# Kernel optimization log

Measured on AMD Instinct MI355X. Metric: run time of the kernel, lower is better.

Reference implementation:

```python
import jax, jax.numpy as jnp
import numpy as np
from jax import lax

C = 8          # bargs.channel
S = 1024       # bargs.test_sidelen
SIGMA = 1.0    # edge_sigma
KS = int(6 * SIGMA + 1)   # 7
PAD = KS // 2             # 3
BW = S // 6               # border_width
LAM, MU, TH = 5.0, 5.0, 1e-4


def _edge_kernel():
    coords = jnp.arange(KS, dtype=jnp.float32) - (KS - 1.0) / 2.0
    g1 = jnp.exp(-coords ** 2 / (2.0 * SIGMA ** 2))
    g1 = g1 / g1.sum()
    g2 = jnp.outer(g1, g1)
    return jnp.broadcast_to(g2, (C, 1, KS, KS))  # depthwise OIHW


def _alpha():
    # max applicable loop index among {row-dist, col-dist}; interior stays 1.
    r = jnp.arange(S)
    g = jnp.where(r < BW, r, jnp.where(S - 1 - r < BW, S - 1 - r, -1))  # [S]
    m = jnp.maximum(g[:, None], g[None, :])                              # [S,S]
    a = jnp.where(m >= 0, m.astype(jnp.float32) / BW, 1.0)
    return a[None, None]  # [1,1,S,S] broadcasts over channels


def _grad_spectrum():
    gv = jnp.array([[-1., -2., -1.], [0., 0., 0.], [1., 2., 1.]], jnp.float32)
    gh = gv.T
    gvf = jnp.fft.fft2(gv, s=(S, S))
    ghf = jnp.fft.fft2(gh, s=(S, S))
    return (jnp.abs(gvf) ** 2 + jnp.abs(ghf) ** 2).astype(jnp.float32)  # real


def _edge_blur(img, kernel, alpha):
    blurred = lax.conv_general_dilated(
        img, kernel, window_strides=(1, 1), padding=[(PAD, PAD), (PAD, PAD)],
        feature_group_count=C, dimension_numbers=('NCHW', 'OIHW', 'NCHW'))
    return alpha * img + (1.0 - alpha) * blurred


def setup_inputs() -> dict:
    key = jax.random.key(0)
    k1, k2 = jax.random.split(key)
    lms = jax.random.uniform(k1, (1, C, S, S), dtype=jnp.float32)
    fuse = jax.random.uniform(k2, (1, C, S, S), dtype=jnp.float32)
    return {"lms": lms, "fuse": fuse}


def reference(lms, fuse):
    kernel = _edge_kernel()
    alpha = _alpha()
    grad = _grad_spectrum()

    lms_fft = jnp.fft.fft2(_edge_blur(lms, kernel, alpha))
    fuse_fft = jnp.fft.fft2(_edge_blur(fuse, kernel, alpha))

    denom = jnp.abs(fuse_fft) ** 2 + LAM + MU * grad      # real [1,C,S,S]
    numer = jnp.conj(fuse_fft) * lms_fft
    psf = jnp.fft.fftshift(jnp.real(jnp.fft.ifft2(numer / denom)), axes=(-2, -1))
    psf = jnp.where(psf < TH, 0.0, psf)                   # [1,C,S,S]

    def crop(p):  # p: [S,S]
        row, col = jnp.unravel_index(jnp.argmax(p), p.shape)
        patch = lax.dynamic_slice(p, (row - 20, col - 20), (41, 41))
        return patch / jnp.sum(patch)

    psf_l = jax.vmap(crop)(psf[0])        # [C,41,41]
    return psf_l[:, None]                 # [C,1,41,41]
```

## Files before the change

kernel.cpp:

```cpp
#include <hip/hip_runtime.h>
#include <math.h>

#define SS 1024
#define NC 8
#define BWD 170
#define THRESH 1e-4f

typedef unsigned long long ull;

__device__ __forceinline__ float2 cmul(float2 a, float2 b) {
    return make_float2(a.x * b.x - a.y * b.y, a.x * b.y + a.y * b.x);
}

#define XS(a) ((a) ^ (((a) >> 4) & 15))

__device__ __forceinline__ int cmap(int kx) {
    if (kx == 0) return 0;
    if (kx == 512) return 1;
    return (kx < 512) ? (kx << 1) : (((1024 - kx) << 1) | 1);
}

template <int DIR>
__device__ __forceinline__ void bfly4(const float2 v[4], float2 r[4]) {
    float2 a = v[0], b = v[1], c = v[2], d = v[3];
    float2 apc = make_float2(a.x + c.x, a.y + c.y);
    float2 amc = make_float2(a.x - c.x, a.y - c.y);
    float2 bpd = make_float2(b.x + d.x, b.y + d.y);
    float2 jb  = make_float2(-(b.y - d.y), b.x - d.x);
    r[0] = make_float2(apc.x + bpd.x, apc.y + bpd.y);
    r[2] = make_float2(apc.x - bpd.x, apc.y - bpd.y);
    if (DIR == -1) {
        r[1] = make_float2(amc.x - jb.x, amc.y - jb.y);
        r[3] = make_float2(amc.x + jb.x, amc.y + jb.y);
    } else {
        r[1] = make_float2(amc.x + jb.x, amc.y + jb.y);
        r[3] = make_float2(amc.x - jb.x, amc.y - jb.y);
    }
}

template <int DIR>
__device__ __forceinline__ void fft1024_reg(float2 v[4], float2* A, float2* B,
                                            int tid, bool sb) {
    float2* dst = A;
    float2* alt = B;
    #pragma unroll
    for (int t = 0; t < 4; ++t) {
        int s = 1 << (2 * t);
        int k = tid & ~(s - 1);
        float2 r[4];
        bfly4<DIR>(v, r);
        float rev = (float)k * (1.0f / 1024.0f);
        float2 w1 = make_float2(__builtin_amdgcn_cosf(rev),
                                (float)DIR * __builtin_amdgcn_sinf(rev));
        float2 w2 = cmul(w1, w1);
        float2 w3 = cmul(w2, w1);
        int base = tid + 3 * k;
        dst[XS(base)]         = r[0];
        dst[XS(base + s)]     = cmul(r[1], w1);
        dst[XS(base + 2 * s)] = cmul(r[2], w2);
        dst[XS(base + 3 * s)] = cmul(r[3], w3);
        __syncthreads();
        v[0] = dst[XS(tid)];
        v[1] = dst[XS(tid + 256)];
        v[2] = dst[XS(tid + 512)];
        v[3] = dst[XS(tid + 768)];
        if (sb) __syncthreads();
        float2* tmp = dst; dst = alt; alt = tmp;
    }
    float2 r[4];
    bfly4<DIR>(v, r);
    v[0] = r[0]; v[1] = r[1]; v[2] = r[2]; v[3] = r[3];
}

template <int DIR>
__device__ __forceinline__ void fft1024_pair(float2 vA[4], float2 vB[4],
                                             float2* A0, float2* A1,
                                             float2* B0, float2* B1,
                                             int tid, bool sb) {
    float2 *dA = A0, *aA = A1, *dB = B0, *aB = B1;
    #pragma unroll
    for (int t = 0; t < 4; ++t) {
        int s = 1 << (2 * t);
        int k = tid & ~(s - 1);
        float rev = (float)k * (1.0f / 1024.0f);
        float2 w1 = make_float2(__builtin_amdgcn_cosf(rev),
                                (float)DIR * __builtin_amdgcn_sinf(rev));
        float2 w2 = cmul(w1, w1);
        float2 w3 = cmul(w2, w1);
        int base = tid + 3 * k;
        float2 rA[4], rB[4];
        bfly4<DIR>(vA, rA);
        bfly4<DIR>(vB, rB);
        dA[XS(base)]         = rA[0];
        dA[XS(base + s)]     = cmul(rA[1], w1);
        dA[XS(base + 2 * s)] = cmul(rA[2], w2);
        dA[XS(base + 3 * s)] = cmul(rA[3], w3);
        dB[XS(base)]         = rB[0];
        dB[XS(base + s)]     = cmul(rB[1], w1);
        dB[XS(base + 2 * s)] = cmul(rB[2], w2);
        dB[XS(base + 3 * s)] = cmul(rB[3], w3);
        __syncthreads();
        vA[0] = dA[XS(tid)];
        vA[1] = dA[XS(tid + 256)];
        vA[2] = dA[XS(tid + 512)];
        vA[3] = dA[XS(tid + 768)];
        vB[0] = dB[XS(tid)];
        vB[1] = dB[XS(tid + 256)];
        vB[2] = dB[XS(tid + 512)];
        vB[3] = dB[XS(tid + 768)];
        if (sb) __syncthreads();
        float2* tmp = dA; dA = aA; aA = tmp;
        tmp = dB; dB = aB; aB = tmp;
    }
    float2 rA[4], rB[4];
    bfly4<DIR>(vA, rA);
    bfly4<DIR>(vB, rB);
    #pragma unroll
    for (int m = 0; m < 4; ++m) { vA[m] = rA[m]; vB[m] = rB[m]; }
}

#define PIDX(r) ((r) + ((r) >> 5))

__global__ __launch_bounds__(256) void blur_fft_kernel(
        const float* __restrict__ lms, const float* __restrict__ fuse,
        float2* __restrict__ Zf) {
    __shared__ float2 bufA[1024];
    __shared__ float2 smemB2[1068];
    float* rowl = (float*)smemB2;
    float* rowf = rowl + 1068;
    int tid = threadIdx.x;
    int g = blockIdx.x;
    int c = g >> 10;
    int y = (g & 7) * 128 + ((g >> 3) & 127);
    const float* L = lms + ((size_t)c << 20);
    const float* F = fuse + ((size_t)c << 20);
    int x0 = tid << 2;

    double e1 = exp(-0.5), e2 = exp(-2.0), e3 = exp(-4.5);
    double sm = 1.0 + 2.0 * (e1 + e2 + e3);
    float w[7] = { (float)(e3 / sm), (float)(e2 / sm), (float)(e1 / sm),
                   (float)(1.0 / sm),
                   (float)(e1 / sm), (float)(e2 / sm), (float)(e3 / sm) };

    bool rowInt = (y >= BWD) && (y <= SS - 1 - BWD);
    bool skipLoads = rowInt && (tid >= 45) && (tid <= 210);
    bool doH = !rowInt || (tid <= 43) || (tid >= 212);

    float4 cl, cf;
    if (skipLoads) {
        cl = *(const float4*)&L[((size_t)y << 10) + x0];
        cf = *(const float4*)&F[((size_t)y << 10) + x0];
    } else {
        float4 lv[7], fv[7];
        #pragma unroll
        for (int r = 0; r < 7; ++r) {
            int gy = y - 3 + r;
            if (gy >= 0 && gy < SS) {
                lv[r] = *(const float4*)&L[((size_t)gy << 10) + x0];
                fv[r] = *(const float4*)&F[((size_t)gy << 10) + x0];
            } else {
                lv[r] = make_float4(0.f, 0.f, 0.f, 0.f);
                fv[r] = make_float4(0.f, 0.f, 0.f, 0.f);
            }
        }
        cl = lv[3]; cf = fv[3];
        #pragma unroll
        for (int j = 0; j < 4; ++j) {
            float a = 0.f, b = 0.f;
            #pragma unroll
            for (int r = 0; r < 7; ++r) {
                a += w[r] * (&lv[r].x)[j];
                b += w[r] * (&fv[r].x)[j];
            }
            rowl[PIDX(3 + x0 + j)] = a;
            rowf[PIDX(3 + x0 + j)] = b;
        }
    }
    if (tid < 3) {
        rowl[PIDX(tid)] = 0.f; rowf[PIDX(tid)] = 0.f;
        rowl[PIDX(1027 + tid)] = 0.f; rowf[PIDX(1027 + tid)] = 0.f;
    }
    __syncthreads();

    float bl[4] = {0.f, 0.f, 0.f, 0.f}, bf[4] = {0.f, 0.f, 0.f, 0.f};
    if (doH) {
        #pragma unroll
        for (int k = 0; k < 4; ++k) {
            float a = 0.f, b = 0.f;
            #pragma unroll
            for (int j = 0; j < 7; ++j) {
                a += w[j] * rowl[PIDX(x0 + k + j)];
                b += w[j] * rowf[PIDX(x0 + k + j)];
            }
            bl[k] = a; bf[k] = b;
        }
    }
    int gyv = (y < BWD) ? y : ((SS - 1 - y) < BWD ? (SS - 1 - y) : -1);
    #pragma unroll
    for (int k = 0; k < 4; ++k) {
        int x = x0 + k;
        int gx = (x < BWD) ? x : ((SS - 1 - x) < BWD ? (SS - 1 - x) : -1);
        int m = gyv > gx ? gyv : gx;
        float a = (m >= 0) ? (float)m / (float)BWD : 1.0f;
        bufA[XS(x)] = make_float2(a * (&cl.x)[k] + (1.0f - a) * bl[k],
                                  a * (&cf.x)[k] + (1.0f - a) * bf[k]);
    }
    __syncthreads();

    float2 v[4];
    #pragma unroll
    for (int m = 0; m < 4; ++m) v[m] = bufA[XS(tid + (m << 8))];
    fft1024_reg<-1>(v, smemB2, bufA, tid, false);

    float2* Zrow = Zf + (((size_t)c << 20) + ((size_t)y << 10));
    #pragma unroll
    for (int r = 0; r < 4; ++r) Zrow[cmap(tid + (r << 8))] = v[r];
}

__global__ __launch_bounds__(256) void fft2_wiener_kernel(
        const float2* __restrict__ Z, float2* __restrict__ Wb) {
    __shared__ float2 rb[4][1024];
    int tid = threadIdx.x;
    int p = blockIdx.x >> 9;
    int b0 = blockIdx.x & 511;
    int i = ((b0 & 7) << 6) | (b0 >> 3);
    int rows[2];
    rows[0] = (i == 0) ? 0 : i;
    rows[1] = (i == 0) ? 512 : 1024 - i;
    bool selfp = (i == 0);
    int slot = (i == 0) ? 0 : (i << 1);

    const float2* Zp0 = Z + ((size_t)(2 * p) << 20);
    const float2* Zp1 = Z + ((size_t)(2 * p + 1) << 20);
    float2 vA[4], vB[4], nA[4], nB[4];
    #pragma unroll
    for (int m = 0; m < 4; ++m) {
        float4 qq = *(const float4*)&Zp0[((size_t)(tid + (m << 8)) << 10) + slot];
        vA[m] = make_float2(qq.x, qq.y);
        nA[m] = make_float2(qq.z, qq.w);
    }
    #pragma unroll
    for (int m = 0; m < 4; ++m) {
        float4 qq = *(const float4*)&Zp1[((size_t)(tid + (m << 8)) << 10) + slot];
        vB[m] = make_float2(qq.x, qq.y);
        nB[m] = make_float2(qq.z, qq.w);
    }

    fft1024_pair<-1>(vA, vB, rb[2], rb[0], rb[3], rb[1], tid, false);
    #pragma unroll
    for (int r = 0; r < 4; ++r) {
        rb[0][XS(tid + (r << 8))] = vA[r];
        rb[1][XS(tid + (r << 8))] = vB[r];
    }
    fft1024_pair<-1>(nA, nB, rb[2], rb[2], rb[3], rb[3], tid, true);
    #pragma unroll
    for (int r = 0; r < 4; ++r) {
        rb[2][XS(tid + (r << 8))] = nA[r];
        rb[3][XS(tid + (r << 8))] = nB[r];
    }
    __syncthreads();

    float2 gout[2][4];
    #pragma unroll
    for (int o = 0; o < 2; ++o) {
        int u = rows[o];
        int po = selfp ? o : (1 - o);
        float cu = __builtin_amdgcn_cosf((float)u * (1.0f / 1024.0f));
        float c2u = 2.0f * cu * cu - 1.0f;
        float hu = 2.0f + 2.0f * cu;
        #pragma unroll
        for (int j = 0; j < 4; ++j) {
            int vv = tid + (j << 8);
            int vn = (1024 - vv) & 1023;
            float cv = __builtin_amdgcn_cosf((float)vv * (1.0f / 1024.0f));
            float c2v = 2.0f * cv * cv - 1.0f;
            float hv = 2.0f + 2.0f * cv;
            float grad = (2.0f - 2.0f * c2v) * hu * hu +
                         (2.0f - 2.0f * c2u) * hv * hv;
            float regs = 5.0f + 5.0f * grad;
            float G0x, G0y, G1x, G1y;
            #pragma unroll
            for (int c = 0; c < 2; ++c) {
                float2 a = rb[o * 2 + c][XS(vv)];
                float2 b = rb[po * 2 + c][XS(vn)];
                float Lx = 0.5f * (a.x + b.x), Ly = 0.5f * (a.y - b.y);
                float Fx = 0.5f * (a.y + b.y), Fy = -0.5f * (a.x - b.x);
                float inv = 1.0f / (Fx * Fx + Fy * Fy + regs);
                float nx = (Fx * Lx + Fy * Ly) * inv;
                float ny = (Fx * Ly - Fy * Lx) * inv;
                if (c == 0) { G0x = nx; G0y = ny; } else { G1x = nx; G1y = ny; }
            }
            gout[o][j] = make_float2(G0x - G1y, G0y + G1x);
        }
    }
    __syncthreads();

    fft1024_pair<1>(gout[0], gout[1], rb[0], rb[2], rb[1], rb[3], tid, false);
    const float isc = 1.0f / 1024.0f;
    #pragma unroll
    for (int o = 0; o < 2; ++o) {
        float2* go = Wb + (((size_t)p << 20) + ((size_t)rows[o] << 10));
        #pragma unroll
        for (int r = 0; r < 4; ++r)
            go[tid + (r << 8)] = make_float2(gout[o][r].x * isc,
                                             gout[o][r].y * isc);
    }
}

__global__ __launch_bounds__(256) void ifft_final_kernel(
        const float2* __restrict__ Wd, float* __restrict__ psf,
        ull* __restrict__ bm) {
    __shared__ float2 bufA[1024];
    __shared__ float2 bufB[1024];
    int tid = threadIdx.x;
    int wv = tid >> 6;
    int p = blockIdx.x >> 9;
    int b0 = blockIdx.x & 511;
    int y0 = (((b0 & 7) << 6) | (b0 >> 3)) << 1;
    const float2* g = Wd + (((size_t)p << 20) + y0);
    float4 q[4];
    #pragma unroll
    for (int m = 0; m < 4; ++m)
        q[m] = *(const float4*)&g[(size_t)(tid + (m << 8)) << 10];

    const float sc = 1.0f / 1024.0f;
    #pragma unroll
    for (int half = 0; half < 2; ++half) {
        int y = y0 + half;
        float2 v[4];
        #pragma unroll
        for (int m = 0; m < 4; ++m)
            v[m] = half ? make_float2(q[m].z, q[m].w)
                        : make_float2(q[m].x, q[m].y);
        fft1024_reg<1>(v, bufA, bufB, tid, false);

        int oy = (y + 512) & 1023;
        float* p0 = psf + (((size_t)(2 * p) << 20) + ((size_t)oy << 10));
        float* p1 = p0 + (1u << 20);
        ull e0 = 0, e1 = 0;
        #pragma unroll
        for (int r = 0; r < 4; ++r) {
            int k = tid + (r << 8);
            float re = v[r].x * sc; re = (re < THRESH) ? 0.0f : re;
            float im = v[r].y * sc; im = (im < THRESH) ? 0.0f : im;
            int ox = (k + 512) & 1023;
            p0[ox] = re;
            p1[ox] = im;
            unsigned int idx = ((unsigned int)oy << 10) | (unsigned int)ox;
            ull c0 = ((ull)__float_as_uint(re) << 32) | (ull)(0xFFFFFFFFu - idx);
            ull c1 = ((ull)__float_as_uint(im) << 32) | (ull)(0xFFFFFFFFu - idx);
            e0 = c0 > e0 ? c0 : e0;
            e1 = c1 > e1 ? c1 : e1;
        }
        #pragma unroll
        for (int off = 32; off > 0; off >>= 1) {
            ull o0 = __shfl_down(e0, off);
            ull o1 = __shfl_down(e1, off);
            e0 = o0 > e0 ? o0 : e0;
            e1 = o1 > e1 ? o1 : e1;
        }
        if ((tid & 63) == 0) {
            bm[((size_t)(2 * p) << 12) + (y << 2) + wv] = e0;
            bm[((size_t)(2 * p + 1) << 12) + (y << 2) + wv] = e1;
        }
    }
}

__global__ __launch_bounds__(256) void crop_kernel(
        const float* __restrict__ psf, const ull* __restrict__ bm,
        float* __restrict__ out) {
    int c = blockIdx.x;
    __shared__ ull rmax[256];
    __shared__ float red[256];
    int tid = threadIdx.x;
    ull e = 0;
    for (int i = tid; i < 4096; i += 256) {
        ull v = bm[((size_t)c << 12) + i];
        e = v > e ? v : e;
    }
    rmax[tid] = e;
    __syncthreads();
    for (int s2 = 128; s2 > 0; s2 >>= 1) {
        if (tid < s2) { ull a = rmax[tid], b = rmax[tid + s2]; rmax[tid] = a > b ? a : b; }
        __syncthreads();
    }
    unsigned int bidx = 0xFFFFFFFFu - (unsigned int)(rmax[0] & 0xFFFFFFFFull);
    int row = (int)(bidx >> 10), col = (int)(bidx & 1023);
    int r0 = row - 20; if (r0 < 0) r0 = 0; if (r0 > SS - 41) r0 = SS - 41;
    int c0 = col - 20; if (c0 < 0) c0 = 0; if (c0 > SS - 41) c0 = SS - 41;
    const float* p = psf + ((size_t)c << 20);
    float local = 0.0f;
    for (int i = tid; i < 1681; i += 256) {
        int rr = i / 41, cc = i - rr * 41;
        local += p[(size_t)(r0 + rr) * SS + c0 + cc];
    }
    red[tid] = local;
    __syncthreads();
    for (int s2 = 128; s2 > 0; s2 >>= 1) {
        if (tid < s2) red[tid] += red[tid + s2];
        __syncthreads();
    }
    float inv = 1.0f / red[0];
    for (int i = tid; i < 1681; i += 256) {
        int rr = i / 41, cc = i - rr * 41;
        out[c * 1681 + i] = p[(size_t)(r0 + rr) * SS + c0 + cc] * inv;
    }
}

extern "C" void kernel_launch(void* const* d_in, const int* in_sizes, int n_in,
                              void* d_out, int out_size, void* d_ws,
                              size_t ws_size, hipStream_t stream) {
    const float* lms = (const float*)d_in[0];
    const float* fuse = (const float*)d_in[1];
    char* ws = (char*)d_ws;
    float2* Zf = (float2*)ws;
    float2* Wb = (float2*)(ws + ((size_t)64 << 20));
    float* psf = (float*)ws;
    ull* bm = (ull*)(ws + ((size_t)33 << 20));
    float* outp = (float*)d_out;

    blur_fft_kernel<<<8192, 256, 0, stream>>>(lms, fuse, Zf);
    fft2_wiener_kernel<<<2048, 256, 0, stream>>>(Zf, Wb);
    ifft_final_kernel<<<2048, 256, 0, stream>>>(Wb, psf, bm);
    crop_kernel<<<8, 256, 0, stream>>>(psf, bm, outp);
}
```

Before: 190.3 us.

## Skip full PSF write; recompute only the cropped rows after argmax

The inverse-FFT kernel now only computes per-row argmax keys and no longer writes the full thresholded PSF planes to memory. A new kernel reads the global argmax and redoes the row inverse FFT for just the 41 rows of the crop window, writing only the 41x41 patch. This removes a large global write in exchange for redundant FFT work, strided column reads, and an extra kernel launch.

```diff
diff --git a/kernel.cpp b/kernel.cpp
--- a/kernel.cpp
+++ b/kernel.cpp
@@ -307,9 +307,8 @@
     }
 }
 
-__global__ __launch_bounds__(256) void ifft_final_kernel(
-        const float2* __restrict__ Wd, float* __restrict__ psf,
-        ull* __restrict__ bm) {
+__global__ __launch_bounds__(256) void ifft_argmax_kernel(
+        const float2* __restrict__ Wd, ull* __restrict__ bm) {
     __shared__ float2 bufA[1024];
     __shared__ float2 bufB[1024];
     int tid = threadIdx.x;
@@ -335,8 +334,6 @@
         fft1024_reg<1>(v, bufA, bufB, tid, false);
 
         int oy = (y + 512) & 1023;
-        float* p0 = psf + (((size_t)(2 * p) << 20) + ((size_t)oy << 10));
-        float* p1 = p0 + (1u << 20);
         ull e0 = 0, e1 = 0;
         #pragma unroll
         for (int r = 0; r < 4; ++r) {
@@ -344,8 +341,6 @@
             float re = v[r].x * sc; re = (re < THRESH) ? 0.0f : re;
             float im = v[r].y * sc; im = (im < THRESH) ? 0.0f : im;
             int ox = (k + 512) & 1023;
-            p0[ox] = re;
-            p1[ox] = im;
             unsigned int idx = ((unsigned int)oy << 10) | (unsigned int)ox;
             ull c0 = ((ull)__float_as_uint(re) << 32) | (ull)(0xFFFFFFFFu - idx);
             ull c1 = ((ull)__float_as_uint(im) << 32) | (ull)(0xFFFFFFFFu - idx);
@@ -366,16 +361,19 @@
     }
 }
 
-__global__ __launch_bounds__(256) void crop_kernel(
-        const float* __restrict__ psf, const ull* __restrict__ bm,
-        float* __restrict__ out) {
-    int c = blockIdx.x;
+__global__ __launch_bounds__(256) void psf_recompute_kernel(
+        const float2* __restrict__ Wd, const ull* __restrict__ bm,
+        float* __restrict__ patch) {
+    __shared__ float2 bufA[1024];
+    __shared__ float2 bufB[1024];
     __shared__ ull rmax[256];
-    __shared__ float red[256];
     int tid = threadIdx.x;
+    int j = blockIdx.x;
+    int c = blockIdx.y;
+
     ull e = 0;
-    for (int i = tid; i < 4096; i += 256) {
-        ull v = bm[((size_t)c << 12) + i];
+    for (int i2 = tid; i2 < 4096; i2 += 256) {
+        ull v = bm[((size_t)c << 12) + i2];
         e = v > e ? v : e;
     }
     rmax[tid] = e;
@@ -388,12 +386,41 @@
     int row = (int)(bidx >> 10), col = (int)(bidx & 1023);
     int r0 = row - 20; if (r0 < 0) r0 = 0; if (r0 > SS - 41) r0 = SS - 41;
     int c0 = col - 20; if (c0 < 0) c0 = 0; if (c0 > SS - 41) c0 = SS - 41;
-    const float* p = psf + ((size_t)c << 20);
+
+    int oy = r0 + j;
+    int y = (oy + 512) & 1023;
+    int p = c >> 1;
+    const float2* g = Wd + (((size_t)p << 20) + y);
+    float2 v[4];
+    #pragma unroll
+    for (int m = 0; m < 4; ++m)
+        v[m] = g[(size_t)(tid + (m << 8)) << 10];
+    fft1024_reg<1>(v, bufA, bufB, tid, false);
+
+    const float sc = 1.0f / 1024.0f;
+    float* prow = patch + ((size_t)c * 41 + j) * 41;
+    #pragma unroll
+    for (int r = 0; r < 4; ++r) {
+        int k = tid + (r << 8);
+        int ox = (k + 512) & 1023;
+        int d = ox - c0;
+        if (d >= 0 && d < 41) {
+            float val = (c & 1) ? v[r].y : v[r].x;
+            val *= sc;
+            val = (val < THRESH) ? 0.0f : val;
+            prow[d] = val;
+        }
+    }
+}
+
+__global__ __launch_bounds__(256) void crop_final_kernel(
+        const float* __restrict__ patch, float* __restrict__ out) {
+    int c = blockIdx.x;
+    __shared__ float red[256];
+    int tid = threadIdx.x;
+    const float* pc = patch + (size_t)c * 1681;
     float local = 0.0f;
-    for (int i = tid; i < 1681; i += 256) {
-        int rr = i / 41, cc = i - rr * 41;
-        local += p[(size_t)(r0 + rr) * SS + c0 + cc];
-    }
+    for (int i = tid; i < 1681; i += 256) local += pc[i];
     red[tid] = local;
     __syncthreads();
     for (int s2 = 128; s2 > 0; s2 >>= 1) {
@@ -401,10 +428,8 @@
         __syncthreads();
     }
     float inv = 1.0f / red[0];
-    for (int i = tid; i < 1681; i += 256) {
-        int rr = i / 41, cc = i - rr * 41;
-        out[c * 1681 + i] = p[(size_t)(r0 + rr) * SS + c0 + cc] * inv;
-    }
+    for (int i = tid; i < 1681; i += 256)
+        out[c * 1681 + i] = pc[i] * inv;
 }
 
 extern "C" void kernel_launch(void* const* d_in, const int* in_sizes, int n_in,
@@ -415,12 +440,13 @@
     char* ws = (char*)d_ws;
     float2* Zf = (float2*)ws;
     float2* Wb = (float2*)(ws + ((size_t)64 << 20));
-    float* psf = (float*)ws;
     ull* bm = (ull*)(ws + ((size_t)33 << 20));
+    float* patch = (float*)(ws + ((size_t)34 << 20));
     float* outp = (float*)d_out;
 
     blur_fft_kernel<<<8192, 256, 0, stream>>>(lms, fuse, Zf);
     fft2_wiener_kernel<<<2048, 256, 0, stream>>>(Zf, Wb);
-    ifft_final_kernel<<<2048, 256, 0, stream>>>(Wb, psf, bm);
-    crop_kernel<<<8, 256, 0, stream>>>(psf, bm, outp);
-}
+    ifft_argmax_kernel<<<2048, 256, 0, stream>>>(Wb, bm);
+    psf_recompute_kernel<<<dim3(41, 8), 256, 0, stream>>>(Wb, bm, patch);
+    crop_final_kernel<<<8, 256, 0, stream>>>(patch, outp);
+}
```

Result: slower. 196.9 us (+3.5%).
